# Kernel tuning notes

Hardware: AMD Instinct MI355X
Metric: run time of the kernel (lower is better)

Reference implementation:

```python
import jax, jax.numpy as jnp
import numpy as np


def _consts():
    # Hypercube vertices: itertools.product([-1,1], repeat=n) order => MSB-first bits.
    def verts(nbits):
        idx = np.arange(2 ** nbits)
        return (((idx[:, None] >> np.arange(nbits - 1, -1, -1)[None, :]) & 1) * 2.0 - 1.0).astype(np.float32)

    hexagrams = verts(6)   # (64, 6)
    q2_verts = verts(2)    # (4, 2)
    q3_verts = verts(3)    # (8, 3)

    # Q2 vertex -> group one-hot, _Q2_TO_GROUP = [2, 1, 1, 0]
    q2_to_group = np.zeros((4, 3), dtype=np.float32)
    for v, g in enumerate([2, 1, 1, 0]):
        q2_to_group[v, g] = 1.0

    # Group anchors: ABSTRACT = mean(hex[63], hex[62]), DYNAMIC = mean(hex[19], hex[21]),
    # CONCRETE = mean(hex[0], hex[8]); then L2-normalized.
    anch = np.stack([
        hexagrams[[63, 62]].mean(0),
        hexagrams[[19, 21]].mean(0),
        hexagrams[[0, 8]].mean(0),
    ]).astype(np.float32)
    anch = anch / np.clip(np.linalg.norm(anch, axis=-1, keepdims=True), 1e-12, None)

    # Walsh-Hadamard popcount masks, pre-divided by their sums -> (64, 3) matrix.
    bits = np.array([bin(i).count('1') for i in range(64)], dtype=np.float32)
    wa = (bits >= 5).astype(np.float32)
    wd = (bits == 3).astype(np.float32)
    wc = (bits <= 1).astype(np.float32)
    wht_mat = np.stack([wa / wa.sum(), wd / wd.sum(), wc / wc.sum()], axis=1)

    return tuple(jnp.asarray(a) for a in (hexagrams, q2_verts, q3_verts, q2_to_group, anch, wht_mat))


def _q3_to_group_init():
    q3_map = np.zeros((8, 3), dtype=np.float32)
    for i in range(8):
        yc = bin(i).count('1')
        if yc == 0:
            q3_map[i, 2] = 1.0
        elif yc == 1:
            q3_map[i, 1] = 1.0
        elif yc == 2:
            q3_map[i, 0] = 0.6
            q3_map[i, 1] = 0.4
        else:
            q3_map[i, 0] = 1.0
    q3_map = q3_map / np.clip(q3_map.sum(axis=1, keepdims=True), 1e-8, None)
    return q3_map


def setup_inputs() -> dict:
    key = jax.random.key(0)
    k_x, k2, k3, k6 = jax.random.split(key, 4)
    B, T, D = 4, 4096, 2048
    s = 1.0 / float(np.sqrt(D))  # torch Linear default init range
    return {
        'x': jax.random.normal(k_x, (B, T, D), dtype=jnp.float32),
        'ln_w': jnp.ones((D,), dtype=jnp.float32),
        'ln_b': jnp.zeros((D,), dtype=jnp.float32),
        'w_q2': jax.random.uniform(k2, (2, D), minval=-s, maxval=s, dtype=jnp.float32),
        'w_q3': jax.random.uniform(k3, (3, D), minval=-s, maxval=s, dtype=jnp.float32),
        'w_q6': jax.random.uniform(k6, (6, D), minval=-s, maxval=s, dtype=jnp.float32),
        'log_temp': jnp.asarray(np.log(0.5), dtype=jnp.float32),
        'log_scale_mix': jnp.zeros((3,), dtype=jnp.float32),
        'q3_to_group': jnp.asarray(_q3_to_group_init()),
        'log_wht_mix': jnp.asarray(-2.0, dtype=jnp.float32),
    }


def _forward(x, ln_w, ln_b, w_q2, w_q3, w_q6, log_temp, log_scale_mix, q3_to_group, log_wht_mix):
    hexa, q2v, q3v, q2g, anch, wht_mat = _consts()

    # LayerNorm (eps = 1e-5, torch default)
    mu = x.mean(-1, keepdims=True)
    var = ((x - mu) ** 2).mean(-1, keepdims=True)
    h = (x - mu) * jax.lax.rsqrt(var + 1e-5) * ln_w + ln_b

    temp = jnp.clip(jnp.exp(log_temp), 0.1, 5.0)

    # Q2 scale: (B,T,2) -> 4 vertices -> 3 groups
    w2 = jax.nn.softmax(jnp.tanh(h @ w_q2.T) @ q2v.T / temp, axis=-1)
    score_q2 = w2 @ q2g

    # Q3 scale: (B,T,3) -> 8 vertices -> learned soft group map
    w3 = jax.nn.softmax(jnp.tanh(h @ w_q3.T) @ q3v.T / temp, axis=-1)
    score_q3 = w3 @ jax.nn.softmax(q3_to_group, axis=-1)

    # Q6 scale: (B,T,6) -> 64 hexagram vertices
    hex_w = jax.nn.softmax(jnp.tanh(h @ w_q6.T) @ hexa.T / temp, axis=-1)
    score_cos = (hex_w @ hexa) @ anch.T            # cosine-sim vs normalized anchors
    score_wht = hex_w @ wht_mat                    # popcount-mask averages
    alpha = jax.nn.sigmoid(log_wht_mix)
    score_q6 = (1.0 - alpha) * score_cos + alpha * score_wht

    mix = jax.nn.softmax(log_scale_mix)
    group_w = jax.nn.softmax(mix[0] * score_q2 + mix[1] * score_q3 + mix[2] * score_q6, axis=-1)

    mg = group_w.mean(axis=(0, 1))
    mh = hex_w.mean(axis=(0, 1))
    lb_loss = jnp.sum(mg * jnp.log(mg + 1e-8)) + 0.1 * jnp.sum(mh * jnp.log(mh + 1e-8))
    return group_w, hex_w, lb_loss


def reference(x, ln_w, ln_b, w_q2, w_q3, w_q6, log_temp, log_scale_mix, q3_to_group, log_wht_mix):
    return _forward(x, ln_w, ln_b, w_q2, w_q3, w_q6, log_temp, log_scale_mix, q3_to_group, log_wht_mix)
```

## Files before the change

kernel.cpp:

```cpp
#include <hip/hip_runtime.h>
#include <math.h>
#include <string.h>

#define D 2048
#define NTOK 16384
#define NROW 11
#define MROWS_U32 (NROW * D / 2)
#define K1_BLOCKS 1024
#define K1_THREADS 512

#define WS_A 0
#define WS_B 16
#define WS_IT 32
#define WS_ALPHA 33
#define WS_MIX 34
#define WS_M3 40
#define WS_MERGED 64
#define WS_PART (WS_MERGED + MROWS_U32)

typedef __fp16 h2 __attribute__((ext_vector_type(2)));

__device__ __forceinline__ float wsum(float v){
#pragma unroll
  for (int m = 1; m < 64; m <<= 1) v += __shfl_xor(v, m, 64);
  return v;
}
__device__ __forceinline__ float wmax(float v){
#pragma unroll
  for (int m = 1; m < 64; m <<= 1) v = fmaxf(v, __shfl_xor(v, m, 64));
  return v;
}
__device__ __forceinline__ float rcp_fast(float x){ return __builtin_amdgcn_rcpf(x); }
__device__ __forceinline__ float tanh_fast(float x){
  float e = __expf(2.0f * x);
  return 1.0f - 2.0f * rcp_fast(e + 1.0f);
}
__device__ __forceinline__ float sload(const float* __restrict__ p){
  return __uint_as_float(__builtin_amdgcn_readfirstlane(__float_as_uint(*p)));
}
__device__ __forceinline__ h2 u2h(unsigned int u){ h2 h; memcpy(&h, &u, 4); return h; }
__device__ __forceinline__ unsigned int h2u(h2 h){ unsigned int u; memcpy(&u, &h, 4); return u; }

__device__ __forceinline__ float fdot2(h2 a, h2 b, float c){
#if __has_builtin(__builtin_amdgcn_fdot2)
  return __builtin_amdgcn_fdot2(a, b, c, false);
#else
  return fmaf((float)a[0], (float)b[0], fmaf((float)a[1], (float)b[1], c));
#endif
}

__global__ __launch_bounds__(256) void k0_prep(
    const float* __restrict__ ln_w, const float* __restrict__ ln_b,
    const float* __restrict__ w_q2, const float* __restrict__ w_q3,
    const float* __restrict__ w_q6,
    const float* __restrict__ log_temp, const float* __restrict__ log_scale_mix,
    const float* __restrict__ q3_to_group, const float* __restrict__ log_wht_mix,
    float* __restrict__ ws)
{
  const int tid = threadIdx.x;
  const int k = blockIdx.x;
  unsigned int* wsu = (unsigned int*)ws;
  if (k < NROW){
    const float* row = (k < 2) ? (w_q2 + (size_t)k * D)
                     : (k < 5) ? (w_q3 + (size_t)(k - 2) * D)
                               : (w_q6 + (size_t)(k - 5) * D);
    float pa = 0.f, pb = 0.f;
    for (int i = tid * 2; i < D; i += 512){
      float w0 = row[i], w1 = row[i + 1];
      h2 h = __builtin_amdgcn_cvt_pkrtz(ln_w[i] * w0, ln_w[i + 1] * w1);
      pa += (float)h[0] + (float)h[1];
      pb = fmaf(ln_b[i], w0, pb);
      pb = fmaf(ln_b[i + 1], w1, pb);
      wsu[WS_MERGED + k * 1024 + i / 2] = h2u(h);
    }
    __shared__ float red[8];
    pa = wsum(pa); pb = wsum(pb);
    if ((tid & 63) == 0){ red[tid >> 6] = pa; red[4 + (tid >> 6)] = pb; }
    __syncthreads();
    if (tid == 0){
      ws[WS_A + k] = red[0] + red[1] + red[2] + red[3];
      ws[WS_B + k] = red[4] + red[5] + red[6] + red[7];
    }
  } else if (tid == 0){
    float t = __expf(log_temp[0]);
    t = fminf(fmaxf(t, 0.1f), 5.0f);
    ws[WS_IT] = 1.0f / t;
    ws[WS_ALPHA] = 1.0f / (1.0f + __expf(-log_wht_mix[0]));
    float m0 = log_scale_mix[0], m1 = log_scale_mix[1], m2 = log_scale_mix[2];
    float mm = fmaxf(m0, fmaxf(m1, m2));
    float e0 = __expf(m0 - mm), e1 = __expf(m1 - mm), e2 = __expf(m2 - mm);
    float inv = 1.0f / (e0 + e1 + e2);
    ws[WS_MIX + 0] = e0 * inv; ws[WS_MIX + 1] = e1 * inv; ws[WS_MIX + 2] = e2 * inv;
    for (int r = 0; r < 8; ++r){
      float v0 = q3_to_group[r*3+0], v1 = q3_to_group[r*3+1], v2 = q3_to_group[r*3+2];
      float mx = fmaxf(v0, fmaxf(v1, v2));
      float f0 = __expf(v0 - mx), f1 = __expf(v1 - mx), f2 = __expf(v2 - mx);
      float iv = 1.0f / (f0 + f1 + f2);
      ws[WS_M3 + r*3 + 0] = f0 * iv;
      ws[WS_M3 + r*3 + 1] = f1 * iv;
      ws[WS_M3 + r*3 + 2] = f2 * iv;
    }
  }
}

__global__ __launch_bounds__(512) void k1_main(
    const float* __restrict__ x, const float* __restrict__ ws,
    float* __restrict__ gout, float* __restrict__ hout, float* __restrict__ part)
{
  __shared__ unsigned int sW[MROWS_U32];
  __shared__ float lred[8][68];
  const int tid  = threadIdx.x;
  const int lane = tid & 63;
  const int wid  = tid >> 6;
  const int blk  = blockIdx.x;
  const int tok0 = blk * 16 + wid * 2;

  const unsigned int* wsu = (const unsigned int*)ws + WS_MERGED;

  const float* xp0 = x + (size_t)tok0 * D + lane * 4;
  const float* xp1 = xp0 + D;
  float4 xa[8], xb[8];
#pragma unroll
  for (int i = 0; i < 8; ++i) xa[i] = *(const float4*)(xp0 + i * 256);
#pragma unroll
  for (int i = 0; i < 8; ++i) xb[i] = *(const float4*)(xp1 + i * 256);

  {
    const uint4* src = (const uint4*)wsu;
    uint4* dst = (uint4*)sW;
#pragma unroll
    for (int i = 0; i < 6; ++i){
      int idx = tid + i * 512;
      if (idx < MROWS_U32 / 4) dst[idx] = src[idx];
    }
  }

  float sum0 = 0.f, sum1 = 0.f, sq0 = 0.f, sq1 = 0.f;
  h2 xah[16], xbh[16];
#pragma unroll
  for (int i = 0; i < 8; ++i){
    float a0 = xa[i].x, a1 = xa[i].y, a2 = xa[i].z, a3 = xa[i].w;
    sum0 += (a0 + a1) + (a2 + a3);
    sq0 = fmaf(a0,a0, fmaf(a1,a1, fmaf(a2,a2, fmaf(a3,a3, sq0))));
    xah[2*i]   = __builtin_amdgcn_cvt_pkrtz(a0, a1);
    xah[2*i+1] = __builtin_amdgcn_cvt_pkrtz(a2, a3);
    float b0 = xb[i].x, b1 = xb[i].y, b2 = xb[i].z, b3 = xb[i].w;
    sum1 += (b0 + b1) + (b2 + b3);
    sq1 = fmaf(b0,b0, fmaf(b1,b1, fmaf(b2,b2, fmaf(b3,b3, sq1))));
    xbh[2*i]   = __builtin_amdgcn_cvt_pkrtz(b0, b1);
    xbh[2*i+1] = __builtin_amdgcn_cvt_pkrtz(b2, b3);
  }
  __syncthreads();

  float t0[NROW], t1[NROW];
#pragma unroll
  for (int r = 0; r < NROW; ++r){ t0[r] = 0.f; t1[r] = 0.f; }
#pragma unroll
  for (int c = 0; c < 8; ++c){
    const unsigned int* wb = sW + (c << 7) + lane * 2;
    const h2 a0 = xah[2*c], a1 = xah[2*c + 1];
    const h2 b0 = xbh[2*c], b1 = xbh[2*c + 1];
#pragma unroll
    for (int k = 0; k < NROW; ++k){
      uint2 wu = *(const uint2*)(wb + (k << 10));
      h2 w0 = u2h(wu.x), w1 = u2h(wu.y);
      t0[k] = fdot2(a1, w1, fdot2(a0, w0, t0[k]));
      t1[k] = fdot2(b1, w1, fdot2(b0, w0, t1[k]));
    }
  }

  sum0 = wsum(sum0); sum1 = wsum(sum1);
  sq0  = wsum(sq0);  sq1  = wsum(sq1);
#pragma unroll
  for (int k = 0; k < NROW; ++k){ t0[k] = wsum(t0[k]); t1[k] = wsum(t1[k]); }

  float a[NROW], bb[NROW];
#pragma unroll
  for (int k = 0; k < NROW; ++k){ a[k] = sload(ws + WS_A + k); bb[k] = sload(ws + WS_B + k); }
  const float it    = sload(ws + WS_IT);
  const float alpha = sload(ws + WS_ALPHA);
  const float mix0 = sload(ws + WS_MIX), mix1 = sload(ws + WS_MIX + 1), mix2 = sload(ws + WS_MIX + 2);
  float M3r[8][3];
#pragma unroll
  for (int r = 0; r < 8; ++r){
#pragma unroll
    for (int g = 0; g < 3; ++g) M3r[r][g] = sload(ws + WS_M3 + r*3 + g);
  }

  float sgn[6];
#pragma unroll
  for (int j = 0; j < 6; ++j) sgn[j] = ((lane >> (5 - j)) & 1) ? 1.0f : -1.0f;
  const float C5 = 0.44721359549995793f;
  const float A0c[6] = { C5,  C5,  C5,  C5,  C5, 0.f };
  const float A1c[6] = {-0.5f, 0.5f, -0.5f, 0.f, 0.f, 0.5f};
  const float A2c[6] = {-C5, -C5, 0.f, -C5, -C5, -C5};
  float cs0 = 0.f, cs1 = 0.f, cs2 = 0.f;
#pragma unroll
  for (int j = 0; j < 6; ++j){
    cs0 = fmaf(sgn[j], A0c[j], cs0);
    cs1 = fmaf(sgn[j], A1c[j], cs1);
    cs2 = fmaf(sgn[j], A2c[j], cs2);
  }
  const int pc = __popc(lane);
  const float w7c = 1.0f / 7.0f;
  float wh0 = (pc >= 5) ? w7c  : 0.f;
  float wh1 = (pc == 3) ? 0.05f: 0.f;
  float wh2 = (pc <= 1) ? w7c  : 0.f;
  const float m60 = (1.f - alpha)*cs0 + alpha*wh0;
  const float m61 = (1.f - alpha)*cs1 + alpha*wh1;
  const float m62 = (1.f - alpha)*cs2 + alpha*wh2;

  float hsum = 0.f, ga0 = 0.f, ga1 = 0.f, ga2 = 0.f;

#pragma unroll
  for (int j = 0; j < 2; ++j){
    const int tok = tok0 + j;
    const float sumj = j ? sum1 : sum0;
    const float sqj  = j ? sq1  : sq0;
    float mean = sumj * (1.0f / D);
    float var  = fmaf(sqj, 1.0f / D, -mean * mean);
    float rr   = rsqrtf(var + 1e-5f);
    float u[NROW];
#pragma unroll
    for (int k = 0; k < NROW; ++k){
      float tk = j ? t1[k] : t0[k];
      float d = fmaf(-mean, a[k], tk);
      u[k] = tanh_fast(fmaf(rr, d, bb[k]));
    }

    float p01 = u[0] + u[1], m01 = u[0] - u[1];
    float l0 = -p01*it, l1 = -m01*it, l2 = m01*it, l3 = p01*it;
    float mx2 = fmaxf(fmaxf(l0, l1), fmaxf(l2, l3));
    float e0 = __expf(l0-mx2), e1 = __expf(l1-mx2), e2 = __expf(l2-mx2), e3 = __expf(l3-mx2);
    float i2 = rcp_fast(e0 + e1 + e2 + e3);
    float s2g0 = e3 * i2, s2g1 = (e1 + e2) * i2, s2g2 = e0 * i2;

    float l3v[8]; float mx3 = -1e30f;
#pragma unroll
    for (int v = 0; v < 8; ++v){
      float acc3 = ((v & 4) ? u[2] : -u[2]) + ((v & 2) ? u[3] : -u[3]) + ((v & 1) ? u[4] : -u[4]);
      l3v[v] = acc3 * it;
      mx3 = fmaxf(mx3, l3v[v]);
    }
    float w3v[8]; float se3 = 0.f;
#pragma unroll
    for (int v = 0; v < 8; ++v){ w3v[v] = __expf(l3v[v] - mx3); se3 += w3v[v]; }
    float i3 = rcp_fast(se3);
    float s3g0 = 0.f, s3g1 = 0.f, s3g2 = 0.f;
#pragma unroll
    for (int v = 0; v < 8; ++v){
      s3g0 = fmaf(w3v[v], M3r[v][0], s3g0);
      s3g1 = fmaf(w3v[v], M3r[v][1], s3g1);
      s3g2 = fmaf(w3v[v], M3r[v][2], s3g2);
    }
    s3g0 *= i3; s3g1 *= i3; s3g2 *= i3;

    float lg = 0.f;
#pragma unroll
    for (int jj = 0; jj < 6; ++jj) lg = fmaf(sgn[jj], u[5 + jj], lg);
    lg *= it;
    float mx6 = wmax(lg);
    float p   = __expf(lg - mx6);
    float se6 = wsum(p);
    float hw  = p * rcp_fast(se6);
    hout[(size_t)tok * 64 + lane] = hw;
    hsum += hw;
    float s6g0 = wsum(hw * m60);
    float s6g1 = wsum(hw * m61);
    float s6g2 = wsum(hw * m62);

    float g0 = mix0*s2g0 + mix1*s3g0 + mix2*s6g0;
    float g1 = mix0*s2g1 + mix1*s3g1 + mix2*s6g1;
    float g2 = mix0*s2g2 + mix1*s3g2 + mix2*s6g2;
    float gm = fmaxf(g0, fmaxf(g1, g2));
    float y0 = __expf(g0-gm), y1 = __expf(g1-gm), y2 = __expf(g2-gm);
    float gi = rcp_fast(y0 + y1 + y2);
    float gw0 = y0*gi, gw1 = y1*gi, gw2 = y2*gi;
    ga0 += gw0; ga1 += gw1; ga2 += gw2;
    if (lane < 3){
      float val = (lane == 0) ? gw0 : (lane == 1) ? gw1 : gw2;
      gout[(size_t)tok * 3 + lane] = val;
    }
  }

  lred[wid][lane] = hsum;
  if (lane < 3){
    float val = (lane == 0) ? ga0 : (lane == 1) ? ga1 : ga2;
    lred[wid][64 + lane] = val;
  }
  __syncthreads();
  if (tid < 67){
    float v = 0.f;
#pragma unroll
    for (int r = 0; r < 8; ++r) v += lred[r][tid];
    part[(size_t)tid * K1_BLOCKS + blk] = v;
  }
}

__global__ __launch_bounds__(1024) void k2_loss(const float* __restrict__ part,
                                                float* __restrict__ lout)
{
  __shared__ float sums[68];
  const int tid = threadIdx.x;
  const int lane = tid & 63;
  const int wid  = tid >> 6;
  for (int jv = wid; jv < 67; jv += 16){
    const float4* p = (const float4*)(part + (size_t)jv * K1_BLOCKS);
    float v = 0.f;
#pragma unroll
    for (int b = 0; b < K1_BLOCKS / 256; ++b){
      float4 q = p[lane + b * 64];
      v += (q.x + q.y) + (q.z + q.w);
    }
    v = wsum(v);
    if (lane == 0) sums[jv] = v;
  }
  __syncthreads();
  if (wid == 0){
    const float inv = 1.0f / (float)NTOK;
    float mh = sums[lane] * inv;
    float term = 0.1f * mh * logf(mh + 1e-8f);
    if (lane < 3){
      float mg = sums[64 + lane] * inv;
      term += mg * logf(mg + 1e-8f);
    }
    float L = wsum(term);
    if (lane == 0) lout[0] = L;
  }
}

extern "C" void kernel_launch(void* const* d_in, const int* in_sizes, int n_in,
                              void* d_out, int out_size, void* d_ws, size_t ws_size,
                              hipStream_t stream)
{
  const float* x             = (const float*)d_in[0];
  const float* ln_w          = (const float*)d_in[1];
  const float* ln_b          = (const float*)d_in[2];
  const float* w_q2          = (const float*)d_in[3];
  const float* w_q3          = (const float*)d_in[4];
  const float* w_q6          = (const float*)d_in[5];
  const float* log_temp      = (const float*)d_in[6];
  const float* log_scale_mix = (const float*)d_in[7];
  const float* q3_to_group   = (const float*)d_in[8];
  const float* log_wht_mix   = (const float*)d_in[9];

  float* out  = (float*)d_out;
  float* gout = out;
  float* hout = out + (size_t)NTOK * 3;
  float* lout = out + (size_t)NTOK * 3 + (size_t)NTOK * 64;
  float* ws   = (float*)d_ws;

  k0_prep<<<12, 256, 0, stream>>>(ln_w, ln_b, w_q2, w_q3, w_q6,
                                  log_temp, log_scale_mix, q3_to_group, log_wht_mix, ws);
  k1_main<<<K1_BLOCKS, K1_THREADS, 0, stream>>>(x, ws, gout, hout, ws + WS_PART);
  k2_loss<<<1, 1024, 0, stream>>>(ws + WS_PART, lout);
}
```

Before: 53.87 us.

## Compute token projections with MFMA 16x16x32 f16 instead of packed fdot2

The main kernel now uses 256 threads per block. Each wave computes a 16-token by 16-row partial product with the MFMA f16 instruction over one quarter of the hidden dimension, with a ones row appended so the row sum comes out of the same product. The partial results go through a shared-memory tile, are reduced across waves, and then feed the per-token softmax epilogue. This removes the many fdot2 operations and the per-row cross-lane shuffle reductions, and it streams x with a software prefetch. The cost is more shared-memory traffic for the weights and the extra tile reduction, plus fewer threads per block.

```diff
diff --git a/kernel.cpp b/kernel.cpp
--- a/kernel.cpp
+++ b/kernel.cpp
@@ -7,7 +7,10 @@
 #define NROW 11
 #define MROWS_U32 (NROW * D / 2)
 #define K1_BLOCKS 1024
-#define K1_THREADS 512
+#define K1_THREADS 256
+#define WROWS 13
+#define WSTRIDE_U 1032
+#define TILE_S 20
 
 #define WS_A 0
 #define WS_B 16
@@ -19,6 +22,8 @@
 #define WS_PART (WS_MERGED + MROWS_U32)
 
 typedef __fp16 h2 __attribute__((ext_vector_type(2)));
+typedef __fp16 h8 __attribute__((ext_vector_type(8)));
+typedef float f32x4 __attribute__((ext_vector_type(4)));
 
 __device__ __forceinline__ float wsum(float v){
 #pragma unroll
@@ -38,16 +43,7 @@
 __device__ __forceinline__ float sload(const float* __restrict__ p){
   return __uint_as_float(__builtin_amdgcn_readfirstlane(__float_as_uint(*p)));
 }
-__device__ __forceinline__ h2 u2h(unsigned int u){ h2 h; memcpy(&h, &u, 4); return h; }
 __device__ __forceinline__ unsigned int h2u(h2 h){ unsigned int u; memcpy(&u, &h, 4); return u; }
-
-__device__ __forceinline__ float fdot2(h2 a, h2 b, float c){
-#if __has_builtin(__builtin_amdgcn_fdot2)
-  return __builtin_amdgcn_fdot2(a, b, c, false);
-#else
-  return fmaf((float)a[0], (float)b[0], fmaf((float)a[1], (float)b[1], c));
-#endif
-}
 
 __global__ __launch_bounds__(256) void k0_prep(
     const float* __restrict__ ln_w, const float* __restrict__ ln_b,
@@ -103,76 +99,77 @@
   }
 }
 
-__global__ __launch_bounds__(512) void k1_main(
+__global__ __launch_bounds__(256) void k1_main(
     const float* __restrict__ x, const float* __restrict__ ws,
     float* __restrict__ gout, float* __restrict__ hout, float* __restrict__ part)
 {
-  __shared__ unsigned int sW[MROWS_U32];
-  __shared__ float lred[8][68];
+  __shared__ unsigned int sW[WROWS * WSTRIDE_U];
+  __shared__ float tile[4][16][TILE_S];
+  __shared__ float lred[4][68];
   const int tid  = threadIdx.x;
   const int lane = tid & 63;
   const int wid  = tid >> 6;
   const int blk  = blockIdx.x;
-  const int tok0 = blk * 16 + wid * 2;
-
-  const unsigned int* wsu = (const unsigned int*)ws + WS_MERGED;
-
-  const float* xp0 = x + (size_t)tok0 * D + lane * 4;
-  const float* xp1 = xp0 + D;
-  float4 xa[8], xb[8];
-#pragma unroll
-  for (int i = 0; i < 8; ++i) xa[i] = *(const float4*)(xp0 + i * 256);
-#pragma unroll
-  for (int i = 0; i < 8; ++i) xb[i] = *(const float4*)(xp1 + i * 256);
+  const int tok0 = blk * 16;
+  const int n = lane & 15;
+  const int q = lane >> 4;
 
   {
-    const uint4* src = (const uint4*)wsu;
-    uint4* dst = (uint4*)sW;
-#pragma unroll
-    for (int i = 0; i < 6; ++i){
-      int idx = tid + i * 512;
-      if (idx < MROWS_U32 / 4) dst[idx] = src[idx];
-    }
-  }
-
-  float sum0 = 0.f, sum1 = 0.f, sq0 = 0.f, sq1 = 0.f;
-  h2 xah[16], xbh[16];
-#pragma unroll
-  for (int i = 0; i < 8; ++i){
-    float a0 = xa[i].x, a1 = xa[i].y, a2 = xa[i].z, a3 = xa[i].w;
-    sum0 += (a0 + a1) + (a2 + a3);
-    sq0 = fmaf(a0,a0, fmaf(a1,a1, fmaf(a2,a2, fmaf(a3,a3, sq0))));
-    xah[2*i]   = __builtin_amdgcn_cvt_pkrtz(a0, a1);
-    xah[2*i+1] = __builtin_amdgcn_cvt_pkrtz(a2, a3);
-    float b0 = xb[i].x, b1 = xb[i].y, b2 = xb[i].z, b3 = xb[i].w;
-    sum1 += (b0 + b1) + (b2 + b3);
-    sq1 = fmaf(b0,b0, fmaf(b1,b1, fmaf(b2,b2, fmaf(b3,b3, sq1))));
-    xbh[2*i]   = __builtin_amdgcn_cvt_pkrtz(b0, b1);
-    xbh[2*i+1] = __builtin_amdgcn_cvt_pkrtz(b2, b3);
-  }
+    const uint4* src = (const uint4*)((const unsigned int*)ws + WS_MERGED);
+    const uint4 ones4 = make_uint4(0x3C003C00u, 0x3C003C00u, 0x3C003C00u, 0x3C003C00u);
+    const uint4 zero4 = make_uint4(0u, 0u, 0u, 0u);
+#pragma unroll
+    for (int j = 0; j < WROWS; ++j){
+      int idx = tid + j * 256;
+      int r = idx >> 8, i = idx & 255;
+      uint4 v = (r < NROW) ? src[r * 256 + i] : ((r == NROW) ? ones4 : zero4);
+      *(uint4*)(sW + r * WSTRIDE_U + i * 4) = v;
+    }
+  }
+
+  const float* xp = x + (size_t)(tok0 + n) * D + wid * 512 + q * 8;
+
+  f32x4 acc = {0.f, 0.f, 0.f, 0.f};
+  float sq = 0.f;
+
+  float4 f0 = *(const float4*)(xp);
+  float4 f1 = *(const float4*)(xp + 4);
+
   __syncthreads();
 
-  float t0[NROW], t1[NROW];
-#pragma unroll
-  for (int r = 0; r < NROW; ++r){ t0[r] = 0.f; t1[r] = 0.f; }
-#pragma unroll
-  for (int c = 0; c < 8; ++c){
-    const unsigned int* wb = sW + (c << 7) + lane * 2;
-    const h2 a0 = xah[2*c], a1 = xah[2*c + 1];
-    const h2 b0 = xbh[2*c], b1 = xbh[2*c + 1];
-#pragma unroll
-    for (int k = 0; k < NROW; ++k){
-      uint2 wu = *(const uint2*)(wb + (k << 10));
-      h2 w0 = u2h(wu.x), w1 = u2h(wu.y);
-      t0[k] = fdot2(a1, w1, fdot2(a0, w0, t0[k]));
-      t1[k] = fdot2(b1, w1, fdot2(b0, w0, t1[k]));
-    }
-  }
-
-  sum0 = wsum(sum0); sum1 = wsum(sum1);
-  sq0  = wsum(sq0);  sq1  = wsum(sq1);
-#pragma unroll
-  for (int k = 0; k < NROW; ++k){ t0[k] = wsum(t0[k]); t1[k] = wsum(t1[k]); }
+  const int wr = (n <= 12) ? n : 12;
+  const unsigned int* wb = sW + wr * WSTRIDE_U + wid * 256 + q * 4;
+
+#pragma unroll
+  for (int s = 0; s < 16; ++s){
+    float4 g0, g1;
+    if (s < 15){
+      g0 = *(const float4*)(xp + (s + 1) * 32);
+      g1 = *(const float4*)(xp + (s + 1) * 32 + 4);
+    }
+    sq = fmaf(f0.x,f0.x, fmaf(f0.y,f0.y, fmaf(f0.z,f0.z, fmaf(f0.w,f0.w, sq))));
+    sq = fmaf(f1.x,f1.x, fmaf(f1.y,f1.y, fmaf(f1.z,f1.z, fmaf(f1.w,f1.w, sq))));
+    h2 p0 = __builtin_amdgcn_cvt_pkrtz(f0.x, f0.y);
+    h2 p1 = __builtin_amdgcn_cvt_pkrtz(f0.z, f0.w);
+    h2 p2 = __builtin_amdgcn_cvt_pkrtz(f1.x, f1.y);
+    h2 p3 = __builtin_amdgcn_cvt_pkrtz(f1.z, f1.w);
+    h8 A;
+    A[0]=p0[0]; A[1]=p0[1]; A[2]=p1[0]; A[3]=p1[1];
+    A[4]=p2[0]; A[5]=p2[1]; A[6]=p3[0]; A[7]=p3[1];
+    uint4 wq = *(const uint4*)(wb + s * 16);
+    h8 B; memcpy(&B, &wq, 16);
+    acc = __builtin_amdgcn_mfma_f32_16x16x32_f16(A, B, acc, 0, 0, 0);
+    f0 = g0; f1 = g1;
+  }
+
+  sq += __shfl_xor(sq, 16, 64);
+  sq += __shfl_xor(sq, 32, 64);
+
+#pragma unroll
+  for (int r = 0; r < 4; ++r) tile[wid][q * 4 + r][n] = acc[r];
+  if (lane < 16) tile[wid][lane][16] = sq;
+
+  __syncthreads();
 
   float a[NROW], bb[NROW];
 #pragma unroll
@@ -212,19 +209,33 @@
 
   float hsum = 0.f, ga0 = 0.f, ga1 = 0.f, ga2 = 0.f;
 
-#pragma unroll
-  for (int j = 0; j < 2; ++j){
-    const int tok = tok0 + j;
-    const float sumj = j ? sum1 : sum0;
-    const float sqj  = j ? sq1  : sq0;
-    float mean = sumj * (1.0f / D);
-    float var  = fmaf(sqj, 1.0f / D, -mean * mean);
+#pragma unroll 1
+  for (int i = 0; i < 4; ++i){
+    const int tl  = wid * 4 + i;
+    const int tok = tok0 + tl;
+
+    float t[12]; float sqv = 0.f;
+#pragma unroll
+    for (int k = 0; k < 12; ++k) t[k] = 0.f;
+#pragma unroll
+    for (int hh = 0; hh < 4; ++hh){
+      const float* row = &tile[hh][tl][0];
+      float4 c0 = *(const float4*)(row);
+      float4 c1 = *(const float4*)(row + 4);
+      float4 c2 = *(const float4*)(row + 8);
+      t[0] += c0.x; t[1] += c0.y; t[2]  += c0.z; t[3]  += c0.w;
+      t[4] += c1.x; t[5] += c1.y; t[6]  += c1.z; t[7]  += c1.w;
+      t[8] += c2.x; t[9] += c2.y; t[10] += c2.z; t[11] += c2.w;
+      sqv += row[16];
+    }
+
+    float mean = t[11] * (1.0f / D);
+    float var  = fmaf(sqv, 1.0f / D, -mean * mean);
     float rr   = rsqrtf(var + 1e-5f);
     float u[NROW];
 #pragma unroll
     for (int k = 0; k < NROW; ++k){
-      float tk = j ? t1[k] : t0[k];
-      float d = fmaf(-mean, a[k], tk);
+      float d = fmaf(-mean, a[k], t[k]);
       u[k] = tanh_fast(fmaf(rr, d, bb[k]));
     }
 
@@ -290,9 +301,7 @@
   }
   __syncthreads();
   if (tid < 67){
-    float v = 0.f;
-#pragma unroll
-    for (int r = 0; r < 8; ++r) v += lred[r][tid];
+    float v = lred[0][tid] + lred[1][tid] + lred[2][tid] + lred[3][tid];
     part[(size_t)tid * K1_BLOCKS + blk] = v;
   }
 }
```

After: 50.45 us. 1.07x faster.
